# Optimization experiments

Hardware: AMD Instinct MI355X
Metric: run time of the kernel (lower is better)

## Reference

```python
import jax, jax.numpy as jnp
import numpy as np

B, S, D = 2, 2048, 1024
H = 8
HD = D // H  # 128
RANK = 4
CONTROL_SCALE = 1.0


def setup_inputs() -> dict:
    key = jax.random.key(0)
    ks = jax.random.split(key, 8)
    sd = 0.02
    return {
        "hidden_states": jax.random.normal(ks[0], (B, S, D), jnp.float32),
        "control_states": jax.random.normal(ks[1], (B, S, D), jnp.float32),
        "Wq": jax.random.normal(ks[2], (D, D), jnp.float32) * sd,
        "Wk": jax.random.normal(ks[3], (D, D), jnp.float32) * sd,
        "Wv": jax.random.normal(ks[4], (D, D), jnp.float32) * sd,
        "Wo": jax.random.normal(ks[5], (D, D), jnp.float32) * sd,
        "bo": jnp.zeros((D,), jnp.float32),
        "lora_down": jax.random.normal(ks[6], (RANK, D), jnp.float32) * sd,
        "lora_up": jax.random.normal(ks[7], (D, RANK), jnp.float32) * sd,
    }


def _split_heads(x):  # [B,S,D] -> [B,H,S,HD]
    return x.reshape(B, S, H, HD).transpose(0, 2, 1, 3)


def reference(hidden_states, control_states, Wq, Wk, Wv, Wo, bo, lora_down, lora_up):
    # q/k/v projections (Linear, no bias); self-attention (encoder_hidden_states=None)
    q = _split_heads(jnp.einsum("bsd,ed->bse", hidden_states, Wq))
    k = _split_heads(jnp.einsum("bsd,ed->bse", hidden_states, Wk))
    v = _split_heads(jnp.einsum("bsd,ed->bse", hidden_states, Wv))
    inv_sqrt_d = 1.0 / jnp.sqrt(jnp.asarray(HD, q.dtype))
    scores = jnp.einsum("bhqd,bhkd->bhqk", q, k) * inv_sqrt_d  # [B,H,S,S]
    probs = jax.nn.softmax(scores, axis=-1)
    attn_out = jnp.einsum("bhqk,bhkd->bhqd", probs, v)  # [B,H,S,HD]
    attn_out = attn_out.transpose(0, 2, 1, 3).reshape(B, S, D)
    # to_out[0] Linear with bias; to_out[1] Dropout is identity at eval
    out = jnp.einsum("bsd,ed->bse", attn_out, Wo) + bo
    # LoRA control injection: up(down(control_states))
    ctrl = jnp.einsum("bsr,er->bse", jnp.einsum("bsd,rd->bsr", control_states, lora_down), lora_up)
    return out + CONTROL_SCALE * ctrl
```

## Files before the change

### kernel.cpp

```cpp
#include <hip/hip_runtime.h>
#include <hip/hip_bf16.h>


typedef __bf16 bf8_t __attribute__((ext_vector_type(8)));
typedef float f32x4 __attribute__((ext_vector_type(4)));
typedef float f32x16 __attribute__((ext_vector_type(16)));
typedef unsigned u32x4 __attribute__((ext_vector_type(4)));

#define MFMA16(a, b, c) __builtin_amdgcn_mfma_f32_16x16x32_bf16((a), (b), (c), 0, 0, 0)
#define MFMA32(a, b, c) __builtin_amdgcn_mfma_f32_32x32x16_bf16((a), (b), (c), 0, 0, 0)

__device__ __forceinline__ void gload_lds16(const void* g, void* l) {
  __builtin_amdgcn_global_load_lds(
      (const __attribute__((address_space(1))) void*)g,
      (__attribute__((address_space(3))) void*)l, 16, 0, 0);
}

__device__ __forceinline__ unsigned pk2(float a, float b) {
  unsigned short ua = __builtin_bit_cast(unsigned short, (__bf16)a);
  unsigned short ub = __builtin_bit_cast(unsigned short, (__bf16)b);
  return (unsigned)ua | ((unsigned)ub << 16);
}

__global__ __launch_bounds__(256) void cvt5_k(
    const float* __restrict__ s0, const float* __restrict__ s1,
    const float* __restrict__ s2, const float* __restrict__ s3,
    const float* __restrict__ s4, __bf16* __restrict__ d0,
    __bf16* __restrict__ d1, __bf16* __restrict__ d2, __bf16* __restrict__ d3,
    __bf16* __restrict__ d4) {
  const int which = blockIdx.y;
  const float* s = (which == 0) ? s0 : (which == 1) ? s1 : (which == 2) ? s2
                   : (which == 3) ? s3 : s4;
  __bf16* d = (which == 0) ? d0 : (which == 1) ? d1 : (which == 2) ? d2
              : (which == 3) ? d3 : d4;
  const int n = (which == 0) ? (4096 * 1024) : (1024 * 1024);
  const int i = (blockIdx.x * 256 + threadIdx.x) * 8;
  if (i >= n) return;
  float4 a = *(const float4*)(s + i);
  float4 b = *(const float4*)(s + i + 4);
  bf8_t r;
  r[0] = (__bf16)a.x; r[1] = (__bf16)a.y; r[2] = (__bf16)a.z; r[3] = (__bf16)a.w;
  r[4] = (__bf16)b.x; r[5] = (__bf16)b.y; r[6] = (__bf16)b.z; r[7] = (__bf16)b.w;
  *(bf8_t*)(d + i) = r;
}

__device__ __forceinline__ void gemm_tile(const __bf16* __restrict__ Abase,
                                          const __bf16* __restrict__ Wbase,
                                          int K, __bf16* sA, __bf16* sB,
                                          f32x4 acc[4][4]) {
  const int tid = threadIdx.x;
  const int wave = tid >> 6, lane = tid & 63;
  const int wr = (wave >> 1) * 64, wc = (wave & 1) * 64;
  const int lrow = lane >> 3, lchunk = lane & 7;

  for (int m = 0; m < 4; ++m)
    for (int n = 0; n < 4; ++n)
      acc[m][n] = f32x4{0.f, 0.f, 0.f, 0.f};

  for (int k0 = 0; k0 < K; k0 += 64) {
    for (int i = 0; i < 4; ++i) {
      const int rbase = i * 32 + wave * 8;
      gload_lds16(Abase + (size_t)(rbase + lrow) * K + k0 + lchunk * 8,
                  sA + rbase * 64);
      gload_lds16(Wbase + (size_t)(rbase + lrow) * K + k0 + lchunk * 8,
                  sB + rbase * 64);
    }
    __syncthreads();

    for (int kk = 0; kk < 2; ++kk) {
      bf8_t af[4], bfr[4];
      const int koff = kk * 32 + (lane >> 4) * 8;
      for (int m = 0; m < 4; ++m)
        af[m] = *(const bf8_t*)&sA[(wr + m * 16 + (lane & 15)) * 64 + koff];
      for (int n = 0; n < 4; ++n)
        bfr[n] = *(const bf8_t*)&sB[(wc + n * 16 + (lane & 15)) * 64 + koff];
      for (int m = 0; m < 4; ++m)
        for (int n = 0; n < 4; ++n)
          acc[m][n] = MFMA16(af[m], bfr[n], acc[m][n]);
    }
    __syncthreads();
  }
}

__global__ __launch_bounds__(256) void gemm_qkv_k(
    const __bf16* __restrict__ X, const __bf16* __restrict__ Wq,
    const __bf16* __restrict__ Wk, const __bf16* __restrict__ Wv,
    __bf16* __restrict__ Qb, __bf16* __restrict__ Kb, __bf16* __restrict__ Vtb) {
  __shared__ __bf16 sA[128 * 64];
  __shared__ __bf16 sB[128 * 64];
  const int z = blockIdx.z;
  const int K = 1024;
  int rowT, colT, Nout;
  const __bf16 *Abase, *Wbase;
  __bf16* C;
  if (z == 2) {
    rowT = blockIdx.x; colT = blockIdx.y; Nout = 4096;
    Abase = Wv + (size_t)rowT * 128 * K;
    Wbase = X + (size_t)colT * 128 * K;
    C = Vtb;
  } else {
    rowT = blockIdx.y; colT = blockIdx.x; Nout = 1024;
    Abase = X + (size_t)rowT * 128 * K;
    Wbase = ((z == 0) ? Wq : Wk) + (size_t)colT * 128 * K;
    C = (z == 0) ? Qb : Kb;
  }
  f32x4 acc[4][4];
  gemm_tile(Abase, Wbase, K, sA, sB, acc);

  const int lane = threadIdx.x & 63, wave = threadIdx.x >> 6;
  const int wr = (wave >> 1) * 64, wc = (wave & 1) * 64;
  const int row0 = rowT * 128 + wr + (lane >> 4) * 4;
  const int col0 = colT * 128 + wc + (lane & 15);
  for (int m = 0; m < 4; ++m)
    for (int n = 0; n < 4; ++n)
      for (int j = 0; j < 4; ++j)
        C[(size_t)(row0 + m * 16 + j) * Nout + col0 + n * 16] = (__bf16)acc[m][n][j];
}

__global__ __launch_bounds__(256) void lora_down_k(
    const float* __restrict__ ctrl, const float* __restrict__ down,
    float* __restrict__ tmp) {
  const int tid = threadIdx.x, wave = tid >> 6, lane = tid & 63;
  const int s = blockIdx.x * 4 + wave;
  const float* cp = ctrl + (size_t)s * 1024 + lane * 16;
  float4 c[4];
  for (int i = 0; i < 4; ++i) c[i] = *(const float4*)(cp + i * 4);
  for (int r = 0; r < 4; ++r) {
    const float* dp = down + r * 1024 + lane * 16;
    float acc = 0.f;
    for (int i = 0; i < 4; ++i) {
      float4 dv = *(const float4*)(dp + i * 4);
      acc += c[i].x * dv.x + c[i].y * dv.y + c[i].z * dv.z + c[i].w * dv.w;
    }
    for (int off = 32; off > 0; off >>= 1) acc += __shfl_xor(acc, off);
    if (lane == 0) tmp[s * 4 + r] = acc;
  }
}

__global__ __launch_bounds__(128) void flash_attn_k(
    const __bf16* __restrict__ Qg, const __bf16* __restrict__ Kg,
    const __bf16* __restrict__ Vtg, __bf16* __restrict__ Op,
    float* __restrict__ ml) {
  const int S = 2048, D = 1024;
  __shared__ __bf16 sK[2][32 * 128];
  __shared__ __bf16 sVt[2][128 * 32];
  __shared__ float sW[2][32];
  const int qt = blockIdx.x, bh = blockIdx.y, z = blockIdx.z;
  const int b = bh >> 3, h = bh & 7;
  const int tid = threadIdx.x, wave = tid >> 6, lane = tid & 63;
  const int l31 = lane & 31, hi = lane >> 5;
  const size_t base = (size_t)b * S * D + (size_t)h * 128;
  const size_t vtbase = (size_t)h * 128 * 4096 + (size_t)b * 2048;
  const int q0 = qt * 64 + wave * 32;
  const int kvbase = z * 1024;

  bf8_t qf[8];
  {
    const float c = 0.08838834764831845f * 1.4426950408889634f;
    const __bf16* qp = Qg + base + (size_t)(q0 + l31) * D + hi * 8;
#pragma unroll
    for (int dc = 0; dc < 8; ++dc) {
      bf8_t v = *(const bf8_t*)(qp + dc * 16);
#pragma unroll
      for (int j = 0; j < 8; ++j) v[j] = (__bf16)((float)v[j] * c);
      qf[dc] = v;
    }
  }

  f32x16 accO[4];
#pragma unroll
  for (int db = 0; db < 4; ++db)
#pragma unroll
    for (int j = 0; j < 16; ++j) accO[db][j] = 0.f;
  float m_ = -1e30f, l_ = 0.f;

  auto stageK = [&](int buf, int kv) {
#pragma unroll
    for (int i = 0; i < 4; ++i) {
      const int r = wave * 16 + i * 4 + (lane >> 4);
      const int gc = (lane & 15) ^ (r & 7);
      gload_lds16(Kg + base + (size_t)(kv + r) * D + gc * 8,
                  &sK[buf][(wave * 16 + i * 4) * 128]);
    }
  };
  auto stageV = [&](int buf, int kv) {
#pragma unroll
    for (int i = 0; i < 4; ++i) {
      const int d = wave * 64 + i * 16 + (lane >> 2);
      const int gc = (lane & 3) ^ (d & 3);
      gload_lds16(Vtg + vtbase + (size_t)d * 4096 + kv + gc * 8,
                  &sVt[buf][(wave * 64 + i * 16) * 32]);
    }
  };

  stageK(0, kvbase);
  stageV(0, kvbase);

  for (int t = 0; t < 32; ++t) {
    const int cur = t & 1;
    __syncthreads();
    if (t < 31) {
      stageK(cur ^ 1, kvbase + (t + 1) * 32);
      stageV(cur ^ 1, kvbase + (t + 1) * 32);
    }

    f32x16 accS;
#pragma unroll
    for (int j = 0; j < 16; ++j) accS[j] = 0.f;
    const __bf16* kb_ = sK[cur];
    const int kr = l31;
#pragma unroll
    for (int dc = 0; dc < 8; ++dc) {
      bf8_t a = *(const bf8_t*)&kb_[kr * 128 + ((2 * dc + hi) ^ (kr & 7)) * 8];
      accS = MFMA32(a, qf[dc], accS);
    }

    float pm = accS[0];
#pragma unroll
    for (int j = 1; j < 16; ++j) pm = fmaxf(pm, accS[j]);
    pm = fmaxf(pm, __shfl_xor(pm, 32));

    if (__ballot(pm > m_ + 8.0f)) {
      const float mn = fmaxf(m_, pm);
      const float sc = exp2f(m_ - mn);
      m_ = mn;
      l_ *= sc;
      if (hi == 0) sW[wave][l31] = sc;
#pragma unroll
      for (int r = 0; r < 16; ++r) {
        const float scr = sW[wave][(r & 3) + 8 * (r >> 2) + 4 * hi];
#pragma unroll
        for (int db = 0; db < 4; ++db) accO[db][r] *= scr;
      }
    }

    float rs = 0.f;
#pragma unroll
    for (int j = 0; j < 16; ++j) {
      const float p = exp2f(accS[j] - m_);
      accS[j] = p;
      rs += p;
    }
    rs += __shfl_xor(rs, 32);
    l_ += rs;

    unsigned pk[4][2];
#pragma unroll
    for (int tq = 0; tq < 4; ++tq) {
      pk[tq][0] = pk2(accS[4 * tq + 0], accS[4 * tq + 1]);
      pk[tq][1] = pk2(accS[4 * tq + 2], accS[4 * tq + 3]);
    }

    const __bf16* vt_ = sVt[cur];
#pragma unroll
    for (int kc = 0; kc < 2; ++kc) {
      const unsigned own0 = hi ? pk[2 * kc + 1][0] : pk[2 * kc][0];
      const unsigned own1 = hi ? pk[2 * kc + 1][1] : pk[2 * kc][1];
      const unsigned snd0 = hi ? pk[2 * kc][0] : pk[2 * kc + 1][0];
      const unsigned snd1 = hi ? pk[2 * kc][1] : pk[2 * kc + 1][1];
      const unsigned rc0 = (unsigned)__shfl_xor((int)snd0, 32);
      const unsigned rc1 = (unsigned)__shfl_xor((int)snd1, 32);
      u32x4 fr;
      fr[0] = hi ? rc0 : own0;
      fr[1] = hi ? rc1 : own1;
      fr[2] = hi ? own0 : rc0;
      fr[3] = hi ? own1 : rc1;
      const bf8_t pa = __builtin_bit_cast(bf8_t, fr);
#pragma unroll
      for (int db = 0; db < 4; ++db) {
        const int dr = db * 32 + l31;
        bf8_t vb = *(const bf8_t*)&vt_[dr * 32 + ((kc * 2 + hi) ^ (dr & 3)) * 8];
        accO[db] = MFMA32(pa, vb, accO[db]);
      }
    }
  }

  const size_t pbase = ((size_t)(z * 16 + bh) * 2048 + q0);
#pragma unroll
  for (int r = 0; r < 16; ++r) {
    const int qr = (r & 3) + 8 * (r >> 2) + 4 * hi;
    __bf16* op = Op + (pbase + qr) * 128 + l31;
#pragma unroll
    for (int db = 0; db < 4; ++db)
      op[db * 32] = (__bf16)(accO[db][r]);
  }
  if (hi == 0) {
    ml[(pbase + l31) * 2 + 0] = m_;
    ml[(pbase + l31) * 2 + 1] = l_;
  }
}

__global__ __launch_bounds__(256) void attn_merge_k(
    const __bf16* __restrict__ Op, const float* __restrict__ ml,
    __bf16* __restrict__ Og) {
  const int bh = blockIdx.x >> 7, qc = blockIdx.x & 127;
  const int t = threadIdx.x;
  const int qr = qc * 16 + (t >> 4);
  const int d0 = (t & 15) * 8;
  const int b = bh >> 3, h = bh & 7;

  const size_t i0 = ((size_t)bh * 2048 + qr);
  const size_t i1 = ((size_t)(16 + bh) * 2048 + qr);
  const float m0 = ml[i0 * 2], l0 = ml[i0 * 2 + 1];
  const float m1 = ml[i1 * 2], l1 = ml[i1 * 2 + 1];
  const float m = fmaxf(m0, m1);
  const float w0 = exp2f(m0 - m), w1 = exp2f(m1 - m);
  const float inv = 1.0f / (l0 * w0 + l1 * w1);

  bf8_t o0 = *(const bf8_t*)(Op + i0 * 128 + d0);
  bf8_t o1 = *(const bf8_t*)(Op + i1 * 128 + d0);
  bf8_t r;
#pragma unroll
  for (int j = 0; j < 8; ++j)
    r[j] = (__bf16)(((float)o0[j] * w0 + (float)o1[j] * w1) * inv);
  *(bf8_t*)(Og + ((size_t)(b * 2048 + qr) * 1024) + h * 128 + d0) = r;
}

__global__ __launch_bounds__(256) void gemm_out_k(
    const __bf16* __restrict__ A, const __bf16* __restrict__ Wo,
    const float* __restrict__ bo, const float* __restrict__ lup,
    const float* __restrict__ tmp, float* __restrict__ out) {
  __shared__ __bf16 sA[128 * 64];
  __shared__ __bf16 sB[128 * 64];
  const int bcol = blockIdx.x, brow = blockIdx.y;
  const int K = 1024, N = 1024;
  f32x4 acc[4][4];
  gemm_tile(A + (size_t)brow * 128 * K, Wo + (size_t)bcol * 128 * K, K, sA, sB, acc);

  const int lane = threadIdx.x & 63, wave = threadIdx.x >> 6;
  const int wr = (wave >> 1) * 64, wc = (wave & 1) * 64;
  for (int n = 0; n < 4; ++n) {
    const int col = bcol * 128 + wc + n * 16 + (lane & 15);
    const float bias = bo[col];
    const float u0 = lup[col * 4 + 0], u1 = lup[col * 4 + 1];
    const float u2 = lup[col * 4 + 2], u3 = lup[col * 4 + 3];
    for (int m = 0; m < 4; ++m)
      for (int j = 0; j < 4; ++j) {
        const int row = brow * 128 + wr + m * 16 + (lane >> 4) * 4 + j;
        const float* t = tmp + row * 4;
        float v = acc[m][n][j] + bias + t[0] * u0 + t[1] * u1 + t[2] * u2 + t[3] * u3;
        out[(size_t)row * N + col] = v;
      }
  }
}

extern "C" void kernel_launch(void* const* d_in, const int* in_sizes, int n_in,
                              void* d_out, int out_size, void* d_ws, size_t ws_size,
                              hipStream_t stream) {
  (void)in_sizes; (void)n_in; (void)out_size; (void)ws_size;
  const float* hs  = (const float*)d_in[0];
  const float* cs  = (const float*)d_in[1];
  const float* Wq  = (const float*)d_in[2];
  const float* Wk  = (const float*)d_in[3];
  const float* Wv  = (const float*)d_in[4];
  const float* Wo  = (const float*)d_in[5];
  const float* bo  = (const float*)d_in[6];
  const float* ldw = (const float*)d_in[7];
  const float* lup = (const float*)d_in[8];
  float* out = (float*)d_out;

  const size_t MD = (size_t)4096 * 1024;
  const size_t WD = (size_t)1024 * 1024;
  __bf16* hsb = (__bf16*)d_ws;
  __bf16* Wqb = hsb + MD;
  __bf16* Wkb = Wqb + WD;
  __bf16* Wvb = Wkb + WD;
  __bf16* Wob = Wvb + WD;
  __bf16* Qb  = Wob + WD;
  __bf16* Kb  = Qb + MD;
  __bf16* Vtb = Kb + MD;
  __bf16* Ab  = Vtb + MD;
  float*  tmp = (float*)(Ab + MD);
  __bf16* Opart = (__bf16*)(tmp + 4096 * 4);
  float*  mlp   = (float*)(Opart + (size_t)2 * 16 * 2048 * 128);

  cvt5_k<<<dim3(2048, 5), 256, 0, stream>>>(hs, Wq, Wk, Wv, Wo,
                                            hsb, Wqb, Wkb, Wvb, Wob);
  gemm_qkv_k<<<dim3(8, 32, 3), 256, 0, stream>>>(hsb, Wqb, Wkb, Wvb, Qb, Kb, Vtb);
  lora_down_k<<<dim3(1024), 256, 0, stream>>>(cs, ldw, tmp);
  flash_attn_k<<<dim3(32, 16, 2), 128, 0, stream>>>(Qb, Kb, Vtb, Opart, mlp);
  attn_merge_k<<<dim3(2048), 256, 0, stream>>>(Opart, mlp, Ab);
  gemm_out_k<<<dim3(8, 32), 256, 0, stream>>>(Ab, Wob, bo, lup, tmp, out);
}
```

Baseline: 169.2 us.

## Halve out-GEMM row tile, precompute attention staging pointers, add MFMA priority hints

The output projection GEMM now uses a templated 64x128 tile, which doubles the number of workgroups from 256 to 512 to improve occupancy across the GPU. In flash attention, the K/V staging addresses are hoisted into precomputed base pointers. The V-transpose LDS swizzle changes to a (dr>>1)&3 pattern to reduce bank conflicts, and s_setprio raises wave priority around the MFMA blocks. In exchange, the output GEMM gets less data reuse per tile, and the swizzle change must stay consistent between the write and read sides.

```diff
diff --git a/kernel.cpp b/kernel.cpp
--- a/kernel.cpp
+++ b/kernel.cpp
@@ -44,37 +44,41 @@
   *(bf8_t*)(d + i) = r;
 }
 
+template <int MR>
 __device__ __forceinline__ void gemm_tile(const __bf16* __restrict__ Abase,
                                           const __bf16* __restrict__ Wbase,
                                           int K, __bf16* sA, __bf16* sB,
-                                          f32x4 acc[4][4]) {
+                                          f32x4 acc[MR][4]) {
   const int tid = threadIdx.x;
   const int wave = tid >> 6, lane = tid & 63;
-  const int wr = (wave >> 1) * 64, wc = (wave & 1) * 64;
+  const int wr = (wave >> 1) * (MR * 16), wc = (wave & 1) * 64;
   const int lrow = lane >> 3, lchunk = lane & 7;
 
-  for (int m = 0; m < 4; ++m)
+  for (int m = 0; m < MR; ++m)
     for (int n = 0; n < 4; ++n)
       acc[m][n] = f32x4{0.f, 0.f, 0.f, 0.f};
 
   for (int k0 = 0; k0 < K; k0 += 64) {
-    for (int i = 0; i < 4; ++i) {
+    for (int i = 0; i < MR; ++i) {
       const int rbase = i * 32 + wave * 8;
       gload_lds16(Abase + (size_t)(rbase + lrow) * K + k0 + lchunk * 8,
                   sA + rbase * 64);
+    }
+    for (int i = 0; i < 4; ++i) {
+      const int rbase = i * 32 + wave * 8;
       gload_lds16(Wbase + (size_t)(rbase + lrow) * K + k0 + lchunk * 8,
                   sB + rbase * 64);
     }
     __syncthreads();
 
     for (int kk = 0; kk < 2; ++kk) {
-      bf8_t af[4], bfr[4];
+      bf8_t af[MR], bfr[4];
       const int koff = kk * 32 + (lane >> 4) * 8;
-      for (int m = 0; m < 4; ++m)
+      for (int m = 0; m < MR; ++m)
         af[m] = *(const bf8_t*)&sA[(wr + m * 16 + (lane & 15)) * 64 + koff];
       for (int n = 0; n < 4; ++n)
         bfr[n] = *(const bf8_t*)&sB[(wc + n * 16 + (lane & 15)) * 64 + koff];
-      for (int m = 0; m < 4; ++m)
+      for (int m = 0; m < MR; ++m)
         for (int n = 0; n < 4; ++n)
           acc[m][n] = MFMA16(af[m], bfr[n], acc[m][n]);
     }
@@ -105,7 +109,7 @@
     C = (z == 0) ? Qb : Kb;
   }
   f32x4 acc[4][4];
-  gemm_tile(Abase, Wbase, K, sA, sB, acc);
+  gemm_tile<4>(Abase, Wbase, K, sA, sB, acc);
 
   const int lane = threadIdx.x & 63, wave = threadIdx.x >> 6;
   const int wr = (wave >> 1) * 64, wc = (wave & 1) * 64;
@@ -174,34 +178,40 @@
     for (int j = 0; j < 16; ++j) accO[db][j] = 0.f;
   float m_ = -1e30f, l_ = 0.f;
 
+  const int krow = wave * 16 + (lane >> 4);
+  const __bf16* kgp = Kg + base + (size_t)(kvbase + krow) * D;
+  __bf16* klds = &sK[0][0] + (wave * 16) * 128;
+  const int vrow = wave * 64 + (lane >> 2);
+  const int vgc = ((lane & 3) ^ ((lane >> 3) & 3)) * 8;
+  const __bf16* vgp = Vtg + vtbase + (size_t)vrow * 4096 + kvbase + vgc;
+  __bf16* vlds = &sVt[0][0] + (wave * 64) * 32;
+
   auto stageK = [&](int buf, int kv) {
+    const __bf16* g = kgp + (size_t)kv * D;
+    __bf16* l = klds + buf * (32 * 128);
 #pragma unroll
     for (int i = 0; i < 4; ++i) {
-      const int r = wave * 16 + i * 4 + (lane >> 4);
-      const int gc = (lane & 15) ^ (r & 7);
-      gload_lds16(Kg + base + (size_t)(kv + r) * D + gc * 8,
-                  &sK[buf][(wave * 16 + i * 4) * 128]);
+      const int gc = (lane & 15) ^ (((lane >> 4) + i * 4) & 7);
+      gload_lds16(g + (size_t)(i * 4) * D + gc * 8, l + i * 4 * 128);
     }
   };
   auto stageV = [&](int buf, int kv) {
-#pragma unroll
-    for (int i = 0; i < 4; ++i) {
-      const int d = wave * 64 + i * 16 + (lane >> 2);
-      const int gc = (lane & 3) ^ (d & 3);
-      gload_lds16(Vtg + vtbase + (size_t)d * 4096 + kv + gc * 8,
-                  &sVt[buf][(wave * 64 + i * 16) * 32]);
-    }
+    const __bf16* g = vgp + kv;
+    __bf16* l = vlds + buf * (128 * 32);
+#pragma unroll
+    for (int i = 0; i < 4; ++i)
+      gload_lds16(g + (size_t)(i * 16) * 4096, l + i * 16 * 32);
   };
 
-  stageK(0, kvbase);
-  stageV(0, kvbase);
+  stageK(0, 0);
+  stageV(0, 0);
 
   for (int t = 0; t < 32; ++t) {
     const int cur = t & 1;
     __syncthreads();
     if (t < 31) {
-      stageK(cur ^ 1, kvbase + (t + 1) * 32);
-      stageV(cur ^ 1, kvbase + (t + 1) * 32);
+      stageK(cur ^ 1, (t + 1) * 32);
+      stageV(cur ^ 1, (t + 1) * 32);
     }
 
     f32x16 accS;
@@ -209,15 +219,17 @@
     for (int j = 0; j < 16; ++j) accS[j] = 0.f;
     const __bf16* kb_ = sK[cur];
     const int kr = l31;
+    __builtin_amdgcn_s_setprio(1);
 #pragma unroll
     for (int dc = 0; dc < 8; ++dc) {
       bf8_t a = *(const bf8_t*)&kb_[kr * 128 + ((2 * dc + hi) ^ (kr & 7)) * 8];
       accS = MFMA32(a, qf[dc], accS);
     }
-
-    float pm = accS[0];
-#pragma unroll
-    for (int j = 1; j < 16; ++j) pm = fmaxf(pm, accS[j]);
+    __builtin_amdgcn_s_setprio(0);
+
+    float pm = fmaxf(accS[0], accS[1]);
+#pragma unroll
+    for (int j = 2; j < 16; ++j) pm = fmaxf(pm, accS[j]);
     pm = fmaxf(pm, __shfl_xor(pm, 32));
 
     if (__ballot(pm > m_ + 8.0f)) {
@@ -266,12 +278,15 @@
       fr[2] = hi ? own0 : rc0;
       fr[3] = hi ? own1 : rc1;
       const bf8_t pa = __builtin_bit_cast(bf8_t, fr);
+      __builtin_amdgcn_s_setprio(1);
 #pragma unroll
       for (int db = 0; db < 4; ++db) {
         const int dr = db * 32 + l31;
-        bf8_t vb = *(const bf8_t*)&vt_[dr * 32 + ((kc * 2 + hi) ^ (dr & 3)) * 8];
+        const int p = (kc * 2 + hi) ^ ((dr >> 1) & 3);
+        bf8_t vb = *(const bf8_t*)&vt_[dr * 32 + p * 8];
         accO[db] = MFMA32(pa, vb, accO[db]);
       }
+      __builtin_amdgcn_s_setprio(0);
     }
   }
 
@@ -320,23 +335,23 @@
     const __bf16* __restrict__ A, const __bf16* __restrict__ Wo,
     const float* __restrict__ bo, const float* __restrict__ lup,
     const float* __restrict__ tmp, float* __restrict__ out) {
-  __shared__ __bf16 sA[128 * 64];
+  __shared__ __bf16 sA[64 * 64];
   __shared__ __bf16 sB[128 * 64];
   const int bcol = blockIdx.x, brow = blockIdx.y;
   const int K = 1024, N = 1024;
-  f32x4 acc[4][4];
-  gemm_tile(A + (size_t)brow * 128 * K, Wo + (size_t)bcol * 128 * K, K, sA, sB, acc);
+  f32x4 acc[2][4];
+  gemm_tile<2>(A + (size_t)brow * 64 * K, Wo + (size_t)bcol * 128 * K, K, sA, sB, acc);
 
   const int lane = threadIdx.x & 63, wave = threadIdx.x >> 6;
-  const int wr = (wave >> 1) * 64, wc = (wave & 1) * 64;
+  const int wr = (wave >> 1) * 32, wc = (wave & 1) * 64;
   for (int n = 0; n < 4; ++n) {
     const int col = bcol * 128 + wc + n * 16 + (lane & 15);
     const float bias = bo[col];
     const float u0 = lup[col * 4 + 0], u1 = lup[col * 4 + 1];
     const float u2 = lup[col * 4 + 2], u3 = lup[col * 4 + 3];
-    for (int m = 0; m < 4; ++m)
+    for (int m = 0; m < 2; ++m)
       for (int j = 0; j < 4; ++j) {
-        const int row = brow * 128 + wr + m * 16 + (lane >> 4) * 4 + j;
+        const int row = brow * 64 + wr + m * 16 + (lane >> 4) * 4 + j;
         const float* t = tmp + row * 4;
         float v = acc[m][n][j] + bias + t[0] * u0 + t[1] * u1 + t[2] * u2 + t[3] * u3;
         out[(size_t)row * N + col] = v;
@@ -380,5 +395,5 @@
   lora_down_k<<<dim3(1024), 256, 0, stream>>>(cs, ldw, tmp);
   flash_attn_k<<<dim3(32, 16, 2), 128, 0, stream>>>(Qb, Kb, Vtb, Opart, mlp);
   attn_merge_k<<<dim3(2048), 256, 0, stream>>>(Opart, mlp, Ab);
-  gemm_out_k<<<dim3(8, 32), 256, 0, stream>>>(Ab, Wob, bo, lup, tmp, out);
-}
+  gemm_out_k<<<dim3(8, 64), 256, 0, stream>>>(Ab, Wob, bo, lup, tmp, out);
+}
```

New measurement: 164.7 us. 2.7% less time.
